# Kernel tuning notes

Measured on AMD Instinct MI355X. Metric: run time of the kernel, lower is better.

The kernel has to match this reference:

```python
import jax, jax.numpy as jnp
import numpy as np

N_ITERS = 200  # matches maxIter=200 in the original QPFunction


def setup_inputs() -> dict:
    key = jax.random.key(0)
    k1, k2, k3 = jax.random.split(key, 3)
    B, M, N = 8192, 128, 64
    A = jax.random.normal(k1, (B, M, N), dtype=jnp.float32)
    x = jax.random.normal(k2, (B, N), dtype=jnp.float32)
    # b > 0 guarantees z = 0 is feasible for A z <= b, so every instance is solvable
    b = jax.random.uniform(k3, (B, M), dtype=jnp.float32)
    Q = jnp.eye(N, dtype=jnp.float32)  # module parameter: self.Q = diag(ones(feature_size))
    return {"Q": Q, "A": A, "x": x, "b": b}


def reference(Q, A, x, b):
    """Batched QP:  min_z 1/2 z^T Q z - x^T z  s.t.  A z <= b.

    Solved via FISTA (accelerated projected gradient ascent) on the dual:
        max_{lam >= 0}  -1/2 (x - A^T lam)^T Q^{-1} (x - A^T lam) - lam^T b + const
    Primal recovery: z = Q^{-1} (x - A^T lam).
    Fully batched and jit-friendly (fixed N_ITERS, lax.scan).
    """
    Qinv = jnp.linalg.inv(Q)  # [n, n], tiny

    # Lipschitz bound for dual gradient: ||A Qinv A^T||_2 <= ||A||_F^2 * ||Qinv||_F
    L = jnp.sum(A * A, axis=(1, 2)) * jnp.linalg.norm(Qinv)  # [B]
    eta = jax.lax.stop_gradient(1.0 / jnp.maximum(L, 1e-12))[:, None]  # [B, 1]

    def primal(lam):
        # z = Qinv (x - A^T lam), shape [B, n]
        return jnp.einsum('nk,bk->bn', Qinv, x - jnp.einsum('bmn,bm->bn', A, lam))

    def step(carry, _):
        lam, y, t = carry
        z = primal(y)                                   # [B, n]
        g = jnp.einsum('bmn,bn->bm', A, z) - b          # dual gradient A z - b, [B, m]
        lam_new = jax.nn.relu(y + eta * g)              # projected ascent step
        t_new = 0.5 * (1.0 + jnp.sqrt(1.0 + 4.0 * t * t))
        y_new = lam_new + ((t - 1.0) / t_new) * (lam_new - lam)
        return (lam_new, y_new, t_new), None

    lam0 = jnp.zeros_like(b)
    t0 = jnp.float32(1.0)
    (lam, _, _), _ = jax.lax.scan(step, (lam0, lam0, t0), None, length=N_ITERS)
    return primal(lam)  # optimal z, [B, n]
```

## Files before the change

kernel.cpp:

```cpp
#include <hip/hip_runtime.h>


constexpr double csqrt_(double x) {
  double g = x * 0.5 + 0.5;
  for (int i = 0; i < 40; ++i) g = 0.5 * (g + x / g);
  return g;
}
struct CoefT { float c[200]; };
constexpr CoefT make_coefs() {
  CoefT T{};
  double t = 1.0;
  for (int k = 0; k < 200; ++k) {
    double tn = 0.5 * (1.0 + csqrt_(1.0 + 4.0 * t * t));
    T.c[k] = (float)((t - 1.0) / tn);
    t = tn;
  }
  return T;
}
__device__ constexpr CoefT kCoef = make_coefs();

__device__ __forceinline__ float dpp_xor1(float v) {
  return __int_as_float(__builtin_amdgcn_update_dpp(0, __float_as_int(v), 0xB1, 0xF, 0xF, true));
}
__device__ __forceinline__ float dpp_xor2(float v) {
  return __int_as_float(__builtin_amdgcn_update_dpp(0, __float_as_int(v), 0x4E, 0xF, 0xF, true));
}
__device__ __forceinline__ float dpp_add_xor1(float v) { return v + dpp_xor1(v); }
__device__ __forceinline__ float dpp_add_xor2(float v) { return v + dpp_xor2(v); }
__device__ __forceinline__ float dpp_add_ror4(float v) {
  return v + __int_as_float(__builtin_amdgcn_update_dpp(0, __float_as_int(v), 0x124, 0xF, 0xF, true));
}
__device__ __forceinline__ float dpp_add_ror8(float v) {
  return v + __int_as_float(__builtin_amdgcn_update_dpp(0, __float_as_int(v), 0x128, 0xF, 0xF, true));
}
__device__ __forceinline__ float dpp_add_hmirror(float v) {
  return v + __int_as_float(__builtin_amdgcn_update_dpp(0, __float_as_int(v), 0x141, 0xF, 0xF, true));
}

__global__ __launch_bounds__(512)
void qp_fista_kernel(const float* __restrict__ A,
                     const float* __restrict__ x,
                     const float* __restrict__ b,
                     float* __restrict__ out) {
  const int batch = blockIdx.x;
  const int tid = threadIdx.x;
  const int w = tid >> 6;

  __shared__ __align__(16) float tile[8192];

  const float* Ag = A + (size_t)batch * 8192;

  {
    const float4* Ag4 = (const float4*)Ag;
    float4* t4 = (float4*)tile;
#pragma unroll
    for (int k = 0; k < 4; ++k) t4[tid + k * 512] = Ag4[tid + k * 512];
  }
  __syncthreads();

  const int rg = tid >> 4;
  const int cs = tid & 15;
  float Ar4[16];
  {
    const float4* t4 = (const float4*)tile;
#pragma unroll
    for (int k = 0; k < 4; ++k) {
      float4 v = t4[(4 * rg + k) * 16 + cs];
      Ar4[4 * k + 0] = v.x; Ar4[4 * k + 1] = v.y;
      Ar4[4 * k + 2] = v.z; Ar4[4 * k + 3] = v.w;
    }
  }
  const int c  = tid >> 3;
  const int rq = tid & 7;
  float Ac[16];
#pragma unroll
  for (int i = 0; i < 16; ++i) Ac[i] = tile[(rq * 16 + i) * 64 + c];

  float ss = 0.f;
#pragma unroll
  for (int i = 0; i < 16; ++i) ss = fmaf(Ar4[i], Ar4[i], ss);
#pragma unroll
  for (int d = 1; d < 64; d <<= 1) ss += __shfl_xor(ss, d, 64);

  __syncthreads();

  float* zbuf = tile;
  float* ybuf = tile + 96;
  float* wsb  = tile + 272;

  if ((tid & 63) == 0) wsb[w] = ss;
  const int myrow = 4 * rg + (tid & 3);
  const float breg = b[(size_t)batch * 128 + myrow];
  const float xreg = x[(size_t)batch * 64 + c];
  if (rq == 0) zbuf[(c >> 4) * 24 + (c & 15)] = xreg;
  __syncthreads();

  float sum8 = 0.f;
#pragma unroll
  for (int i = 0; i < 8; ++i) sum8 += wsb[i];
  const float eta = 1.0f / fmaxf(8.0f * sum8, 1e-12f);
  const float yb0 = eta * breg;

  const float4* zs = (const float4*)(zbuf + (cs >> 2) * 24 + (cs & 3) * 4);
  const float4* ys = (const float4*)(ybuf + rq * 20);
  float* ywr = ybuf + w * 20 + 4 * (rg & 3) + (tid & 3);
  const bool ywrite = ((tid & 12) == 0);
  float* zwr = zbuf + (c >> 4) * 24 + (c & 15);
  const bool sel0 = (tid & 1), sel1 = (tid & 2);

  float lam = 0.f, y = 0.f;

#pragma unroll 2
  for (int it = 0; it < 199; ++it) {
    const float coef = kCoef.c[it];

    __builtin_amdgcn_s_setprio(1);
    float4 zz = *zs;
    float a0 = Ar4[0] * zz.x, a1 = Ar4[4] * zz.x, a2 = Ar4[8] * zz.x, a3 = Ar4[12] * zz.x;
    a0 = fmaf(Ar4[1], zz.y, a0);  a1 = fmaf(Ar4[5], zz.y, a1);
    a2 = fmaf(Ar4[9], zz.y, a2);  a3 = fmaf(Ar4[13], zz.y, a3);
    a0 = fmaf(Ar4[2], zz.z, a0);  a1 = fmaf(Ar4[6], zz.z, a1);
    a2 = fmaf(Ar4[10], zz.z, a2); a3 = fmaf(Ar4[14], zz.z, a3);
    a0 = fmaf(Ar4[3], zz.w, a0);  a1 = fmaf(Ar4[7], zz.w, a1);
    a2 = fmaf(Ar4[11], zz.w, a2); a3 = fmaf(Ar4[15], zz.w, a3);
    float u01 = sel0 ? a1 : a0, v01 = sel0 ? a0 : a1;
    u01 += dpp_xor1(v01);
    float u23 = sel0 ? a3 : a2, v23 = sel0 ? a2 : a3;
    u23 += dpp_xor1(v23);
    float s2 = sel1 ? u23 : u01, t2 = sel1 ? u01 : u23;
    s2 += dpp_xor2(t2);
    s2 = dpp_add_ror4(s2);
    s2 = dpp_add_ror8(s2);
    float ln = fmaxf(0.f, fmaf(eta, s2, y - yb0));
    float yn = fmaf(coef, ln - lam, ln);
    __builtin_amdgcn_s_setprio(0);
    lam = ln; y = yn;
    if (ywrite) *ywr = yn;
    __syncthreads();

    __builtin_amdgcn_s_setprio(1);
    float q0 = 0.f, q1 = 0.f;
#pragma unroll
    for (int j = 0; j < 4; ++j) {
      float4 yy = ys[j];
      q0 = fmaf(Ac[4 * j + 0], yy.x, q0);
      q1 = fmaf(Ac[4 * j + 1], yy.y, q1);
      q0 = fmaf(Ac[4 * j + 2], yy.z, q0);
      q1 = fmaf(Ac[4 * j + 3], yy.w, q1);
    }
    float s = q0 + q1;
    s = dpp_add_xor1(s);
    s = dpp_add_xor2(s);
    s = dpp_add_hmirror(s);
    __builtin_amdgcn_s_setprio(0);
    if (rq == 0) *zwr = xreg - s;
    __syncthreads();
  }

  {
    float4 zz = *zs;
    float a0 = Ar4[0] * zz.x, a1 = Ar4[4] * zz.x, a2 = Ar4[8] * zz.x, a3 = Ar4[12] * zz.x;
    a0 = fmaf(Ar4[1], zz.y, a0);  a1 = fmaf(Ar4[5], zz.y, a1);
    a2 = fmaf(Ar4[9], zz.y, a2);  a3 = fmaf(Ar4[13], zz.y, a3);
    a0 = fmaf(Ar4[2], zz.z, a0);  a1 = fmaf(Ar4[6], zz.z, a1);
    a2 = fmaf(Ar4[10], zz.z, a2); a3 = fmaf(Ar4[14], zz.z, a3);
    a0 = fmaf(Ar4[3], zz.w, a0);  a1 = fmaf(Ar4[7], zz.w, a1);
    a2 = fmaf(Ar4[11], zz.w, a2); a3 = fmaf(Ar4[15], zz.w, a3);
    float u01 = sel0 ? a1 : a0, v01 = sel0 ? a0 : a1;
    u01 += dpp_xor1(v01);
    float u23 = sel0 ? a3 : a2, v23 = sel0 ? a2 : a3;
    u23 += dpp_xor1(v23);
    float s2 = sel1 ? u23 : u01, t2 = sel1 ? u01 : u23;
    s2 += dpp_xor2(t2);
    s2 = dpp_add_ror4(s2);
    s2 = dpp_add_ror8(s2);
    float ln = fmaxf(0.f, fmaf(eta, s2, y - yb0));
    if (ywrite) *ywr = ln;
    __syncthreads();

    float q0 = 0.f, q1 = 0.f;
#pragma unroll
    for (int j = 0; j < 4; ++j) {
      float4 yy = ys[j];
      q0 = fmaf(Ac[4 * j + 0], yy.x, q0);
      q1 = fmaf(Ac[4 * j + 1], yy.y, q1);
      q0 = fmaf(Ac[4 * j + 2], yy.z, q0);
      q1 = fmaf(Ac[4 * j + 3], yy.w, q1);
    }
    float s = q0 + q1;
    s = dpp_add_xor1(s);
    s = dpp_add_xor2(s);
    s = dpp_add_hmirror(s);
    if (rq == 0) *zwr = xreg - s;
    __syncthreads();
  }

  if (tid < 64) {
    out[(size_t)batch * 64 + tid] = zbuf[(tid >> 4) * 24 + (tid & 15)];
  }
}

extern "C" void kernel_launch(void* const* d_in, const int* in_sizes, int n_in,
                              void* d_out, int out_size, void* d_ws, size_t ws_size,
                              hipStream_t stream) {
  const float* A = (const float*)d_in[1];
  const float* x = (const float*)d_in[2];
  const float* b = (const float*)d_in[3];
  float* out = (float*)d_out;
  qp_fista_kernel<<<dim3(8192), dim3(512), 0, stream>>>(A, x, b, out);
}
```

Before: 980.4 us.

## Compute A^T y partials per wave via readlane broadcast instead of LDS y exchange

Each wave now keeps its own 16 rows of A (one column per lane) and broadcasts the wave-local y values with readlane, which yields per-wave partial sums of A^T y without first writing y to shared memory. The partials are stored to a padded LDS buffer and reduced across the 8 waves with DPP adds. The two barriers per iteration remain, but the y write/read exchange through LDS is replaced by a partial-sum exchange. In return each thread issues 16 scalar readlanes per iteration, which adds VALU-to-SALU dependency latency to the critical path.

```diff
diff --git a/kernel.cpp b/kernel.cpp
--- a/kernel.cpp
+++ b/kernel.cpp
@@ -45,6 +45,7 @@
   const int batch = blockIdx.x;
   const int tid = threadIdx.x;
   const int w = tid >> 6;
+  const int lane = tid & 63;
 
   __shared__ __align__(16) float tile[8192];
 
@@ -70,11 +71,9 @@
       Ar4[4 * k + 2] = v.z; Ar4[4 * k + 3] = v.w;
     }
   }
-  const int c  = tid >> 3;
-  const int rq = tid & 7;
-  float Ac[16];
-#pragma unroll
-  for (int i = 0; i < 16; ++i) Ac[i] = tile[(rq * 16 + i) * 64 + c];
+  float Ac1[16];
+#pragma unroll
+  for (int i = 0; i < 16; ++i) Ac1[i] = tile[(16 * w + i) * 64 + lane];
 
   float ss = 0.f;
 #pragma unroll
@@ -85,14 +84,15 @@
   __syncthreads();
 
   float* zbuf = tile;
-  float* ybuf = tile + 96;
-  float* wsb  = tile + 272;
+  float* pbuf = tile + 96;
+  float* wsb  = tile + 680;
 
   if ((tid & 63) == 0) wsb[w] = ss;
   const int myrow = 4 * rg + (tid & 3);
   const float breg = b[(size_t)batch * 128 + myrow];
-  const float xreg = x[(size_t)batch * 64 + c];
-  if (rq == 0) zbuf[(c >> 4) * 24 + (c & 15)] = xreg;
+  const int bcol = tid >> 3, bslot = tid & 7;
+  const float xg = x[(size_t)batch * 64 + bcol];
+  if (tid < 64) zbuf[(tid >> 4) * 24 + (tid & 15)] = x[(size_t)batch * 64 + tid];
   __syncthreads();
 
   float sum8 = 0.f;
@@ -102,10 +102,10 @@
   const float yb0 = eta * breg;
 
   const float4* zs = (const float4*)(zbuf + (cs >> 2) * 24 + (cs & 3) * 4);
-  const float4* ys = (const float4*)(ybuf + rq * 20);
-  float* ywr = ybuf + w * 20 + 4 * (rg & 3) + (tid & 3);
-  const bool ywrite = ((tid & 12) == 0);
-  float* zwr = zbuf + (c >> 4) * 24 + (c & 15);
+  float* pwr = pbuf + lane * 9 + w;
+  const float* prd = pbuf + bcol * 9 + bslot;
+  float* bzw = zbuf + (bcol >> 4) * 24 + (bcol & 15);
+  const bool bwrite = (bslot == 0);
   const bool sel0 = (tid & 1), sel1 = (tid & 2);
 
   float lam = 0.f, y = 0.f;
@@ -133,27 +133,22 @@
     s2 = dpp_add_ror8(s2);
     float ln = fmaxf(0.f, fmaf(eta, s2, y - yb0));
     float yn = fmaf(coef, ln - lam, ln);
+    lam = ln; y = yn;
+    float p = 0.f;
+#pragma unroll
+    for (int j = 0; j < 16; ++j) {
+      int yi = __builtin_amdgcn_readlane(__float_as_int(yn), 16 * (j >> 2) + (j & 3));
+      p = fmaf(__int_as_float(yi), Ac1[j], p);
+    }
     __builtin_amdgcn_s_setprio(0);
-    lam = ln; y = yn;
-    if (ywrite) *ywr = yn;
-    __syncthreads();
-
-    __builtin_amdgcn_s_setprio(1);
-    float q0 = 0.f, q1 = 0.f;
-#pragma unroll
-    for (int j = 0; j < 4; ++j) {
-      float4 yy = ys[j];
-      q0 = fmaf(Ac[4 * j + 0], yy.x, q0);
-      q1 = fmaf(Ac[4 * j + 1], yy.y, q1);
-      q0 = fmaf(Ac[4 * j + 2], yy.z, q0);
-      q1 = fmaf(Ac[4 * j + 3], yy.w, q1);
-    }
-    float s = q0 + q1;
-    s = dpp_add_xor1(s);
-    s = dpp_add_xor2(s);
-    s = dpp_add_hmirror(s);
-    __builtin_amdgcn_s_setprio(0);
-    if (rq == 0) *zwr = xreg - s;
+    *pwr = p;
+    __syncthreads();
+
+    float pv = *prd;
+    pv = dpp_add_xor1(pv);
+    pv = dpp_add_xor2(pv);
+    pv = dpp_add_hmirror(pv);
+    if (bwrite) *bzw = xg - pv;
     __syncthreads();
   }
 
@@ -175,23 +170,19 @@
     s2 = dpp_add_ror4(s2);
     s2 = dpp_add_ror8(s2);
     float ln = fmaxf(0.f, fmaf(eta, s2, y - yb0));
-    if (ywrite) *ywr = ln;
-    __syncthreads();
-
-    float q0 = 0.f, q1 = 0.f;
-#pragma unroll
-    for (int j = 0; j < 4; ++j) {
-      float4 yy = ys[j];
-      q0 = fmaf(Ac[4 * j + 0], yy.x, q0);
-      q1 = fmaf(Ac[4 * j + 1], yy.y, q1);
-      q0 = fmaf(Ac[4 * j + 2], yy.z, q0);
-      q1 = fmaf(Ac[4 * j + 3], yy.w, q1);
+    float p = 0.f;
+#pragma unroll
+    for (int j = 0; j < 16; ++j) {
+      int yi = __builtin_amdgcn_readlane(__float_as_int(ln), 16 * (j >> 2) + (j & 3));
+      p = fmaf(__int_as_float(yi), Ac1[j], p);
     }
-    float s = q0 + q1;
-    s = dpp_add_xor1(s);
-    s = dpp_add_xor2(s);
-    s = dpp_add_hmirror(s);
-    if (rq == 0) *zwr = xreg - s;
+    *pwr = p;
+    __syncthreads();
+    float pv = *prd;
+    pv = dpp_add_xor1(pv);
+    pv = dpp_add_xor2(pv);
+    pv = dpp_add_hmirror(pv);
+    if (bwrite) *bzw = xg - pv;
     __syncthreads();
   }
 
```

Measured after the change: 1.341 ms. +36.7%, slower.
